# Kernel tuning notes

Measured on AMD Instinct MI355X. Metric: run time of the kernel, lower is better.

The kernel has to match this reference:

```python
import jax, jax.numpy as jnp
import numpy as np

B, N, C, H, D, K = 4, 8192, 384, 12, 2, 256
M = N // K          # 32 members per cluster
CH = C // H         # 32 head dim


def setup_inputs() -> dict:
    key = jax.random.key(0)
    ks = jax.random.split(key, 8)
    pos = jax.random.uniform(ks[0], (B, N, D), jnp.float32) * 100.0
    feat = jax.random.normal(ks[1], (B, N, C), jnp.float32)
    # each batch's points partitioned into K clusters of M members (a permutation)
    perms = jax.vmap(lambda kk: jax.random.permutation(kk, N))(jax.random.split(ks[2], B))
    member_idx = perms.reshape(B * K, M).astype(jnp.int32)               # z x m
    batch_idx = jnp.broadcast_to(
        jnp.repeat(jnp.arange(B, dtype=jnp.int32), K)[:, None], (B * K, M))
    w = 0.02
    qkv_w = jax.random.normal(ks[3], (3 * C, C), jnp.float32) * w
    qkv_b = jnp.zeros((3 * C,), jnp.float32)
    pos_w = jax.random.normal(ks[4], (H, D), jnp.float32) * w
    pos_b = jnp.zeros((H,), jnp.float32)
    proj_w = jax.random.normal(ks[5], (C, C), jnp.float32) * w
    proj_b = jnp.zeros((C,), jnp.float32)
    return dict(pos=pos, feat=feat, member_idx=member_idx, batch_idx=batch_idx,
                qkv_w=qkv_w, qkv_b=qkv_b, pos_w=pos_w, pos_b=pos_b,
                proj_w=proj_w, proj_b=proj_b, k=K)


def reference(pos, feat, member_idx, batch_idx, qkv_w, qkv_b, pos_w, pos_b,
              proj_w, proj_b, k):
    # attend_means=True, mask=None, cluster_score=None, q_subsample_idx=None path
    b, n, c = feat.shape
    d = pos.shape[2]
    h = pos_w.shape[0]
    ch = c // h
    z, m = member_idx.shape
    scale = ch ** -0.5

    qkv = feat @ qkv_w.T + qkv_b            # b,n,3c
    q = qkv[..., :c]                        # b,n,c
    kv = qkv[..., c:]                       # b,n,2c

    pos_orig = pos
    pos_n = pos / jnp.max(pos.reshape(-1, d), axis=0)   # per-coordinate max norm

    # irregular gather of kv / pos per cluster member
    kv_g = kv[batch_idx, member_idx]        # z,m,2c
    pos_g = pos_n[batch_idx, member_idx]    # z,m,d

    # cluster_score=None, mask=None -> uniform weights 1/m (mean over members)
    kv_mean = jnp.mean(kv_g, axis=1).reshape(b, k, 2, h, ch)
    pos_mean = jnp.mean(pos_g, axis=1).reshape(b, k, d)

    key_ = kv_mean[:, :, 0].transpose(0, 2, 1, 3)   # b,h,k,ch
    v = kv_mean[:, :, 1].transpose(0, 2, 1, 3)      # b,h,k,ch
    qh = q.reshape(b, n, h, ch).transpose(0, 2, 1, 3) * scale  # b,h,n,ch

    attn = jnp.einsum('bhnc,bhkc->bhnk', qh, key_)  # b,h,n,k
    rel_pos = pos_mean[:, None, :, :] - pos_orig[:, :, None, :]  # b,n,k,d
    pos_bias = jnp.einsum('bnkd,hd->bhnk', rel_pos, pos_w) + pos_b[None, :, None, None]
    attn = jax.nn.softmax(attn + pos_bias, axis=-1)

    out = jnp.einsum('bhnk,bhkc->bnhc', attn, v).reshape(b, n, c)
    return out @ proj_w.T + proj_b
```

## Files before the change

### kernel.cpp

```cpp
#include <hip/hip_runtime.h>

typedef __attribute__((ext_vector_type(8))) short bf16x8;
typedef __attribute__((ext_vector_type(4))) float f32x4;

#define MFMA16(a,b,c) __builtin_amdgcn_mfma_f32_16x16x32_bf16((a),(b),(c),0,0,0)

__device__ __forceinline__ float b2f(unsigned short u){
  union { unsigned u; float f; } x; x.u = ((unsigned)u) << 16; return x.f;
}
__device__ __forceinline__ unsigned short f2b(float f){
  union { float f; unsigned u; } x; x.f = f;
  unsigned r = x.u + 0x7FFFu + ((x.u >> 16) & 1u);
  return (unsigned short)(r >> 16);
}
__device__ __forceinline__ unsigned pk_rne(float a, float b){
  unsigned ua = __float_as_uint(a), ub = __float_as_uint(b);
  ua += 0x7FFFu + ((ua >> 16) & 1u);
  ub += 0x7FFFu + ((ub >> 16) & 1u);
  return __builtin_amdgcn_perm(ub, ua, 0x07060302u);
}
__device__ __forceinline__ unsigned pk_trunc(float a, float b){
  return __builtin_amdgcn_perm(__float_as_uint(b), __float_as_uint(a), 0x07060302u);
}
__device__ __forceinline__ bf16x8 mk8(unsigned a, unsigned b, unsigned c, unsigned d){
  union { uint4 u; bf16x8 h; } x; x.u = make_uint4(a,b,c,d); return x.h;
}
__device__ __forceinline__ int permp(int cl){
  return (cl & 0xE0) | (((cl >> 2) & 3) << 3) | (((cl >> 4) & 1) << 2) | (cl & 3);
}

typedef __attribute__((address_space(3))) unsigned int lds_u32;
typedef const __attribute__((address_space(1))) unsigned int glb_u32;
__device__ __forceinline__ void gl_lds16(const void* g, void* l){
  __builtin_amdgcn_global_load_lds((glb_u32*)g, (lds_u32*)l, 16, 0, 0);
}

__global__ __launch_bounds__(256) void cvt_kernel(const float* __restrict__ in,
                                                  unsigned short* __restrict__ o, long n8){
  long i = (long)blockIdx.x*256 + threadIdx.x;
  if (i >= n8) return;
  const float4* p = (const float4*)(in + i*8);
  float4 a = p[0], b = p[1];
  *(uint4*)(o + i*8) = make_uint4(pk_rne(a.x,a.y), pk_rne(a.z,a.w),
                                  pk_rne(b.x,b.y), pk_rne(b.z,b.w));
}

__global__ __launch_bounds__(256) void posmax_kernel(const float* __restrict__ pos,
                                                     unsigned* __restrict__ pmax){
  int i = blockIdx.x*256 + threadIdx.x;
  float4 v = ((const float4*)pos)[i];
  float m0 = fmaxf(v.x, v.z), m1 = fmaxf(v.y, v.w);
  #pragma unroll
  for (int off = 32; off >= 1; off >>= 1){
    m0 = fmaxf(m0, __shfl_xor(m0, off, 64));
    m1 = fmaxf(m1, __shfl_xor(m1, off, 64));
  }
  if ((threadIdx.x & 63) == 0){
    atomicMax(&pmax[0], __float_as_uint(m0));
    atomicMax(&pmax[1], __float_as_uint(m1));
  }
}

__global__ __launch_bounds__(192) void cluster_means_kernel(
    const float* __restrict__ feat, const float* __restrict__ pos,
    const int* __restrict__ member_idx, const int* __restrict__ batch_idx,
    unsigned short* __restrict__ fm, float* __restrict__ pm)
{
  int z = blockIdx.x, t = threadIdx.x;
  __shared__ int bases[32];
  if (t < 32) bases[t] = batch_idx[z*32 + t]*8192 + member_idx[z*32 + t];
  __syncthreads();
  float a0 = 0.f, a1 = 0.f, p = 0.f;
  for (int m = 0; m < 32; m++){
    const float* row = feat + (long)bases[m]*384;
    a0 += row[t];
    a1 += row[t+192];
    if (t < 2) p += pos[(long)bases[m]*2 + t];
  }
  fm[(long)z*384 + t]       = f2b(a0 * (1.f/32.f));
  fm[(long)z*384 + t + 192] = f2b(a1 * (1.f/32.f));
  if (t < 2) pm[z*2 + t] = p * (1.f/32.f);
}

__global__ __launch_bounds__(256) void bias_kernel(
    const float* __restrict__ pm, const float* __restrict__ pmaxf,
    const float* __restrict__ pos_w, const float* __restrict__ pos_b,
    unsigned short* __restrict__ wt)
{
  int idx = blockIdx.x*256 + threadIdx.x;
  int kc = idx & 255;
  int bh = idx >> 8;
  int h = bh % 12;
  float p0 = pm[((bh/12)*256 + kc)*2]   / pmaxf[0];
  float p1 = pm[((bh/12)*256 + kc)*2+1] / pmaxf[1];
  float bias = p0*pos_w[h*2] + p1*pos_w[h*2+1] + pos_b[h];
  wt[(bh << 8) + permp(kc)] = f2b(exp2f(bias * 1.44269504088896340f));
}

__global__ __launch_bounds__(256) void gemm_kv_kernel(
    const unsigned short* __restrict__ A, const unsigned short* __restrict__ W,
    const float* __restrict__ bias, unsigned short* __restrict__ kh,
    unsigned short* __restrict__ vt, const unsigned short* __restrict__ wt)
{
  __shared__ unsigned short As[64*64];
  __shared__ unsigned short Ws[128*64];
  const int N = 768, K = 384;
  int mt = blockIdx.x / 6, nt = blockIdx.x - mt*6;
  int m0 = mt << 6, n0 = nt << 7;
  int tid = threadIdx.x;
  int lane = tid & 63, wave = tid >> 6;
  int wr = (wave >> 1) << 5, wc = (wave & 1) << 6;
  int l15 = lane & 15, quad = lane >> 4;
  int sw = l15 & 7;
  int srow = tid >> 3, sc8 = tid & 7;

  f32x4 acc[2][4];
  #pragma unroll
  for (int i = 0; i < 2; i++)
    #pragma unroll
    for (int j = 0; j < 4; j++) acc[i][j] = (f32x4){0.f,0.f,0.f,0.f};

  for (int k0 = 0; k0 < K; k0 += 64){
    __syncthreads();
    #pragma unroll
    for (int it = 0; it < 2; it++){
      int r = srow + it*32;
      int gc8 = sc8 ^ (r & 7);
      gl_lds16(A + (long)(m0+r)*K + k0 + gc8*8, As + it*2048 + wave*512);
    }
    #pragma unroll
    for (int it = 0; it < 4; it++){
      int r = srow + it*32;
      int gc8 = sc8 ^ (r & 7);
      gl_lds16(W + (long)(n0+r)*K + k0 + gc8*8, Ws + it*2048 + wave*512);
    }
    __syncthreads();
    #pragma unroll
    for (int kk = 0; kk < 2; kk++){
      bf16x8 af[2], bfr[4];
      #pragma unroll
      for (int i = 0; i < 2; i++)
        af[i] = *(const bf16x8*)(As + (wr + i*16 + l15)*64 + (((kk<<2)+quad) ^ sw)*8);
      #pragma unroll
      for (int j = 0; j < 4; j++)
        bfr[j] = *(const bf16x8*)(Ws + (wc + j*16 + l15)*64 + (((kk<<2)+quad) ^ sw)*8);
      #pragma unroll
      for (int i = 0; i < 2; i++)
        #pragma unroll
        for (int j = 0; j < 4; j++)
          acc[i][j] = MFMA16(af[i], bfr[j], acc[i][j]);
    }
  }

  #pragma unroll
  for (int j = 0; j < 4; j++){
    int col = n0 + wc + j*16 + l15;
    float bv = bias[col];
    #pragma unroll
    for (int i = 0; i < 2; i++){
      int row0 = m0 + wr + i*16 + quad*4;
      #pragma unroll
      for (int r = 0; r < 4; r++){
        float v = acc[i][j][r] + bv;
        int row = row0 + r;
        int b = row >> 8, cl = row & 255;
        if (col < 384){
          int h = col >> 5, ch = col & 31;
          kh[((((long)b*12 + h)*256 + cl)*32) + ch] = f2b(v);
        } else {
          int cn = col - 384;
          int h = cn >> 5, ch = cn & 31;
          int pp = permp(cl);
          int c8 = (pp >> 3) ^ (ch & 7);
          float w = b2f(wt[(((long)b*12 + h) << 8) + pp]);
          vt[(((long)b*12 + h)*32 + ch)*256 + c8*8 + (pp & 7)] = f2b(v * w);
        }
      }
    }
  }
}

template<int OUT_F32, int AF32>
__global__ __launch_bounds__(256) void gemm_fn_kernel(
    const void* __restrict__ Av, const unsigned short* __restrict__ W,
    const float* __restrict__ bias, void* __restrict__ Cv, float out_scale)
{
  __shared__ unsigned short As[64*72];
  __shared__ unsigned short Ws[384*64];
  const int K = 384, N = 384;
  int m0 = blockIdx.x << 6;
  int tid = threadIdx.x;
  int lane = tid & 63, wave = tid >> 6;
  int l15 = lane & 15, quad = lane >> 4;
  int sw = l15 & 7;
  int srow = tid >> 3, sc8 = tid & 7;

  f32x4 acc[4][6];
  #pragma unroll
  for (int i = 0; i < 4; i++)
    #pragma unroll
    for (int j = 0; j < 6; j++) acc[i][j] = (f32x4){0.f,0.f,0.f,0.f};

  for (int k0 = 0; k0 < K; k0 += 64){
    __syncthreads();
    if (AF32){
      const float* Af = (const float*)Av;
      #pragma unroll
      for (int it = 0; it < 4; it++){
        int r = (tid >> 4) + it*16;
        int c4 = tid & 15;
        float4 v = *(const float4*)(Af + (long)(m0+r)*K + k0 + c4*4);
        *(uint2*)(As + r*72 + c4*4) = make_uint2(pk_rne(v.x,v.y), pk_rne(v.z,v.w));
      }
    } else {
      const unsigned short* A = (const unsigned short*)Av;
      #pragma unroll
      for (int it = 0; it < 2; it++){
        int r = srow + it*32;
        int gc8 = sc8 ^ (r & 7);
        gl_lds16(A + (long)(m0+r)*K + k0 + gc8*8, As + it*2048 + wave*512);
      }
    }
    #pragma unroll
    for (int it = 0; it < 12; it++){
      int r = srow + it*32;
      int gc8 = sc8 ^ (r & 7);
      gl_lds16(W + (long)r*K + k0 + gc8*8, Ws + it*2048 + wave*512);
    }
    __syncthreads();
    #pragma unroll
    for (int kk = 0; kk < 2; kk++){
      bf16x8 af[4];
      #pragma unroll
      for (int i = 0; i < 4; i++){
        int r = i*16 + l15;
        if (AF32) af[i] = *(const bf16x8*)(As + r*72 + ((kk<<2)+quad)*8);
        else      af[i] = *(const bf16x8*)(As + r*64 + (((kk<<2)+quad) ^ sw)*8);
      }
      #pragma unroll
      for (int j = 0; j < 6; j++){
        bf16x8 bfr = *(const bf16x8*)(Ws + (wave*96 + j*16 + l15)*64 + (((kk<<2)+quad) ^ sw)*8);
        #pragma unroll
        for (int i = 0; i < 4; i++)
          acc[i][j] = MFMA16(af[i], bfr, acc[i][j]);
      }
    }
  }

  #pragma unroll
  for (int j = 0; j < 6; j++){
    int col = wave*96 + j*16 + l15;
    float bv = bias[col];
    #pragma unroll
    for (int i = 0; i < 4; i++){
      int row0 = m0 + i*16 + quad*4;
      #pragma unroll
      for (int r = 0; r < 4; r++){
        float v = (acc[i][j][r] + bv) * out_scale;
        if (OUT_F32) ((float*)Cv)[(long)(row0+r)*N + col] = v;
        else ((unsigned short*)Cv)[(long)(row0+r)*N + col] = f2b(v);
      }
    }
  }
}

__global__ __launch_bounds__(256) void attn_kernel(
    const unsigned short* __restrict__ qs,
    const unsigned short* __restrict__ kh,
    const unsigned short* __restrict__ vt,
    const unsigned short* __restrict__ wt,
    unsigned short* __restrict__ ao)
{
  __shared__ unsigned short keyS[256*32];
  __shared__ unsigned short vTS[32*256];
  __shared__ unsigned short wS[256];

  int bid = blockIdx.x;
  int chunk = bid & 127;
  int h = (bid >> 7) % 12;
  int b = bid / (128*12);
  int bh = b*12 + h;
  int n0 = chunk << 6;
  int tid = threadIdx.x, lane = tid & 63, wave = tid >> 6;
  int l15 = lane & 15, quad = lane >> 4;
  int sw = l15 & 7;

  const unsigned short* khb = kh + (long)bh*8192;
  const unsigned short* vtb = vt + (long)bh*8192;
  #pragma unroll
  for (int it = 0; it < 4; it++){
    gl_lds16(khb + it*2048 + tid*8, keyS + it*2048 + wave*512);
    gl_lds16(vtb + it*2048 + tid*8, vTS  + it*2048 + wave*512);
  }
  if (tid < 32) *(uint4*)(wS + tid*8) = *(const uint4*)(wt + ((long)bh << 8) + tid*8);
  __syncthreads();

  int tok0 = n0 + wave*16;
  bf16x8 aq = *(const bf16x8*)(qs + ((long)b*8192 + tok0 + l15)*384 + h*32 + quad*8);

  f32x4 S[16];
  #pragma unroll
  for (int kb = 0; kb < 16; kb++){
    bf16x8 bk = *(const bf16x8*)(keyS + (kb*16 + l15)*32 + quad*8);
    f32x4 z = {0.f,0.f,0.f,0.f};
    S[kb] = MFMA16(bk, aq, z);
  }

  #pragma unroll
  for (int kb = 0; kb < 16; kb++)
    #pragma unroll
    for (int c = 0; c < 4; c++) S[kb][c] = exp2f(S[kb][c]);

  f32x4 o0 = {0.f,0.f,0.f,0.f}, o1 = {0.f,0.f,0.f,0.f}, os = {0.f,0.f,0.f,0.f};
  #pragma unroll
  for (int ks = 0; ks < 8; ks++){
    bf16x8 pf = mk8(pk_trunc(S[2*ks][0],   S[2*ks][1]),
                    pk_trunc(S[2*ks][2],   S[2*ks][3]),
                    pk_trunc(S[2*ks+1][0], S[2*ks+1][1]),
                    pk_trunc(S[2*ks+1][2], S[2*ks+1][3]));
    int c8 = (4*ks + quad) ^ sw;
    bf16x8 a0 = *(const bf16x8*)(vTS + l15*256      + c8*8);
    bf16x8 a1 = *(const bf16x8*)(vTS + (16+l15)*256 + c8*8);
    bf16x8 wf = *(const bf16x8*)(wS + ks*32 + quad*8);
    o0 = MFMA16(a0, pf, o0);
    o1 = MFMA16(a1, pf, o1);
    os = MFMA16(wf, pf, os);
  }
  float inv = 1.f / os[0];
  long obase = ((long)b*8192 + tok0 + l15)*384 + h*32 + quad*4;
  unsigned q0 = pk_rne(o0[0]*inv, o0[1]*inv), q1 = pk_rne(o0[2]*inv, o0[3]*inv);
  unsigned q2 = pk_rne(o1[0]*inv, o1[1]*inv), q3 = pk_rne(o1[2]*inv, o1[3]*inv);
  *(uint2*)(ao + obase)      = make_uint2(q0, q1);
  *(uint2*)(ao + obase + 16) = make_uint2(q2, q3);
}

extern "C" void kernel_launch(void* const* d_in, const int* in_sizes, int n_in,
                              void* d_out, int out_size, void* d_ws, size_t ws_size,
                              hipStream_t stream)
{
  const float* pos      = (const float*)d_in[0];
  const float* feat     = (const float*)d_in[1];
  const int* member_idx = (const int*)d_in[2];
  const int* batch_idx  = (const int*)d_in[3];
  const float* qkv_w    = (const float*)d_in[4];
  const float* qkv_b    = (const float*)d_in[5];
  const float* pos_w    = (const float*)d_in[6];
  const float* pos_b    = (const float*)d_in[7];
  const float* proj_w   = (const float*)d_in[8];
  const float* proj_b   = (const float*)d_in[9];
  float* out = (float*)d_out;

  char* ws = (char*)d_ws;
  float* pmax           = (float*)ws;
  float* pm             = (float*)(ws + 256);
  unsigned short* fm    = (unsigned short*)(ws + 8704);
  unsigned short* kh    = (unsigned short*)(ws + 795136);
  unsigned short* vt    = (unsigned short*)(ws + 1581568);
  unsigned short* wt    = (unsigned short*)(ws + 2368000);
  unsigned short* q_s   = (unsigned short*)(ws + 2417152);
  unsigned short* ao    = (unsigned short*)(ws + 27582976);
  unsigned short* qkvwb = (unsigned short*)(ws + 52748800);
  unsigned short* projwb= (unsigned short*)(ws + 53633536);

  hipMemsetAsync(pmax, 0, 8, stream);
  posmax_kernel<<<64, 256, 0, stream>>>(pos, (unsigned*)pmax);
  cvt_kernel<<<216, 256, 0, stream>>>(qkv_w, qkvwb, 55296);
  cvt_kernel<<<72, 256, 0, stream>>>(proj_w, projwb, 18432);
  cluster_means_kernel<<<1024, 192, 0, stream>>>(feat, pos, member_idx, batch_idx, fm, pm);
  bias_kernel<<<48, 256, 0, stream>>>(pm, pmax, pos_w, pos_b, wt);
  gemm_kv_kernel<<<96, 256, 0, stream>>>(fm, qkvwb + 384*384, qkv_b + 384, kh, vt, wt);
  gemm_fn_kernel<0,1><<<512, 256, 0, stream>>>(feat, qkvwb, qkv_b, q_s,
                                               0.17677669529663687f * 1.44269504088896340f);
  attn_kernel<<<6144, 256, 0, stream>>>(q_s, kh, vt, wt, ao);
  gemm_fn_kernel<1,0><<<512, 256, 0, stream>>>(ao, projwb, proj_b, out, 1.0f);
}
```

Baseline: 226.1 us.

## Persistent attention blocks, smaller GEMM k-tile, vectorized cluster-mean gather

The attention kernel now launches one block per (batch, head, 512-token slice) and loops over 8 token chunks. This amortizes the shared-memory load of the key/value tiles, and the next chunk's q fragment is prefetched during the current one. The GEMM k-tile shrinks from 64 to 32 with a 4-way swizzle, cutting LDS footprint to raise occupancy at the cost of twice as many barriers. Cluster means now process two clusters per block using float4 loads and packed bf16 stores.

```diff
diff --git a/kernel.cpp b/kernel.cpp
--- a/kernel.cpp
+++ b/kernel.cpp
@@ -66,20 +66,26 @@
     const int* __restrict__ member_idx, const int* __restrict__ batch_idx,
     unsigned short* __restrict__ fm, float* __restrict__ pm)
 {
-  int z = blockIdx.x, t = threadIdx.x;
-  __shared__ int bases[32];
-  if (t < 32) bases[t] = batch_idx[z*32 + t]*8192 + member_idx[z*32 + t];
+  int t = threadIdx.x;
+  int g = t / 96, tl = t - g*96;
+  int z = blockIdx.x*2 + g;
+  __shared__ int bases[2][32];
+  if (tl < 32) bases[g][tl] = batch_idx[z*32 + tl]*8192 + member_idx[z*32 + tl];
   __syncthreads();
-  float a0 = 0.f, a1 = 0.f, p = 0.f;
+  float4 a = {0.f,0.f,0.f,0.f};
+  float p = 0.f;
+  const float4* f4 = (const float4*)feat;
+  #pragma unroll 4
   for (int m = 0; m < 32; m++){
-    const float* row = feat + (long)bases[m]*384;
-    a0 += row[t];
-    a1 += row[t+192];
-    if (t < 2) p += pos[(long)bases[m]*2 + t];
-  }
-  fm[(long)z*384 + t]       = f2b(a0 * (1.f/32.f));
-  fm[(long)z*384 + t + 192] = f2b(a1 * (1.f/32.f));
-  if (t < 2) pm[z*2 + t] = p * (1.f/32.f);
+    int row = bases[g][m];
+    float4 v = f4[(long)row*96 + tl];
+    a.x += v.x; a.y += v.y; a.z += v.z; a.w += v.w;
+    if (tl < 2) p += pos[(long)row*2 + tl];
+  }
+  unsigned d0 = pk_rne(a.x*(1.f/32.f), a.y*(1.f/32.f));
+  unsigned d1 = pk_rne(a.z*(1.f/32.f), a.w*(1.f/32.f));
+  *(uint2*)(fm + (long)z*384 + tl*4) = make_uint2(d0, d1);
+  if (tl < 2) pm[z*2 + tl] = p * (1.f/32.f);
 }
 
 __global__ __launch_bounds__(256) void bias_kernel(
@@ -185,15 +191,15 @@
     const void* __restrict__ Av, const unsigned short* __restrict__ W,
     const float* __restrict__ bias, void* __restrict__ Cv, float out_scale)
 {
-  __shared__ unsigned short As[64*72];
-  __shared__ unsigned short Ws[384*64];
+  __shared__ unsigned short As[64*32];
+  __shared__ unsigned short Ws[384*32];
   const int K = 384, N = 384;
   int m0 = blockIdx.x << 6;
   int tid = threadIdx.x;
   int lane = tid & 63, wave = tid >> 6;
   int l15 = lane & 15, quad = lane >> 4;
-  int sw = l15 & 7;
-  int srow = tid >> 3, sc8 = tid & 7;
+  int sw3 = l15 & 3;
+  int sr = tid >> 2, sc = tid & 3;
 
   f32x4 acc[4][6];
   #pragma unroll
@@ -201,49 +207,37 @@
     #pragma unroll
     for (int j = 0; j < 6; j++) acc[i][j] = (f32x4){0.f,0.f,0.f,0.f};
 
-  for (int k0 = 0; k0 < K; k0 += 64){
+  for (int k0 = 0; k0 < K; k0 += 32){
     __syncthreads();
     if (AF32){
       const float* Af = (const float*)Av;
-      #pragma unroll
-      for (int it = 0; it < 4; it++){
-        int r = (tid >> 4) + it*16;
-        int c4 = tid & 15;
-        float4 v = *(const float4*)(Af + (long)(m0+r)*K + k0 + c4*4);
-        *(uint2*)(As + r*72 + c4*4) = make_uint2(pk_rne(v.x,v.y), pk_rne(v.z,v.w));
-      }
+      int gc = sc ^ (sr & 3);
+      const float4* src = (const float4*)(Af + (long)(m0+sr)*K + k0 + gc*8);
+      float4 v0 = src[0], v1 = src[1];
+      *(uint4*)(As + sr*32 + sc*8) = make_uint4(pk_rne(v0.x,v0.y), pk_rne(v0.z,v0.w),
+                                                pk_rne(v1.x,v1.y), pk_rne(v1.z,v1.w));
     } else {
       const unsigned short* A = (const unsigned short*)Av;
-      #pragma unroll
-      for (int it = 0; it < 2; it++){
-        int r = srow + it*32;
-        int gc8 = sc8 ^ (r & 7);
-        gl_lds16(A + (long)(m0+r)*K + k0 + gc8*8, As + it*2048 + wave*512);
-      }
-    }
-    #pragma unroll
-    for (int it = 0; it < 12; it++){
-      int r = srow + it*32;
-      int gc8 = sc8 ^ (r & 7);
-      gl_lds16(W + (long)r*K + k0 + gc8*8, Ws + it*2048 + wave*512);
+      int gc = sc ^ (sr & 3);
+      gl_lds16(A + (long)(m0+sr)*K + k0 + gc*8, As + wave*512);
+    }
+    #pragma unroll
+    for (int it = 0; it < 6; it++){
+      int r = it*64 + sr;
+      int gc = sc ^ (r & 3);
+      gl_lds16(W + (long)r*K + k0 + gc*8, Ws + it*2048 + wave*512);
     }
     __syncthreads();
-    #pragma unroll
-    for (int kk = 0; kk < 2; kk++){
-      bf16x8 af[4];
-      #pragma unroll
-      for (int i = 0; i < 4; i++){
-        int r = i*16 + l15;
-        if (AF32) af[i] = *(const bf16x8*)(As + r*72 + ((kk<<2)+quad)*8);
-        else      af[i] = *(const bf16x8*)(As + r*64 + (((kk<<2)+quad) ^ sw)*8);
-      }
-      #pragma unroll
-      for (int j = 0; j < 6; j++){
-        bf16x8 bfr = *(const bf16x8*)(Ws + (wave*96 + j*16 + l15)*64 + (((kk<<2)+quad) ^ sw)*8);
-        #pragma unroll
-        for (int i = 0; i < 4; i++)
-          acc[i][j] = MFMA16(af[i], bfr, acc[i][j]);
-      }
+    bf16x8 af[4];
+    #pragma unroll
+    for (int i = 0; i < 4; i++)
+      af[i] = *(const bf16x8*)(As + (i*16 + l15)*32 + (quad ^ sw3)*8);
+    #pragma unroll
+    for (int j = 0; j < 6; j++){
+      bf16x8 bfr = *(const bf16x8*)(Ws + (wave*96 + j*16 + l15)*32 + (quad ^ sw3)*8);
+      #pragma unroll
+      for (int i = 0; i < 4; i++)
+        acc[i][j] = MFMA16(af[i], bfr, acc[i][j]);
     }
   }
 
@@ -276,11 +270,10 @@
   __shared__ unsigned short wS[256];
 
   int bid = blockIdx.x;
-  int chunk = bid & 127;
-  int h = (bid >> 7) % 12;
-  int b = bid / (128*12);
-  int bh = b*12 + h;
-  int n0 = chunk << 6;
+  int part = bid & 15;
+  int bh = bid >> 4;
+  int h = bh % 12;
+  int b = bh / 12;
   int tid = threadIdx.x, lane = tid & 63, wave = tid >> 6;
   int l15 = lane & 15, quad = lane >> 4;
   int sw = l15 & 7;
@@ -293,45 +286,52 @@
     gl_lds16(vtb + it*2048 + tid*8, vTS  + it*2048 + wave*512);
   }
   if (tid < 32) *(uint4*)(wS + tid*8) = *(const uint4*)(wt + ((long)bh << 8) + tid*8);
+
+  const unsigned short* qrow = qs + ((long)b*8192 + part*512 + wave*16 + l15)*384 + h*32 + quad*8;
+  unsigned short* aorow = ao + ((long)b*8192 + part*512 + wave*16 + l15)*384 + h*32 + quad*4;
+
+  bf16x8 aq = *(const bf16x8*)qrow;
   __syncthreads();
 
-  int tok0 = n0 + wave*16;
-  bf16x8 aq = *(const bf16x8*)(qs + ((long)b*8192 + tok0 + l15)*384 + h*32 + quad*8);
-
-  f32x4 S[16];
-  #pragma unroll
-  for (int kb = 0; kb < 16; kb++){
-    bf16x8 bk = *(const bf16x8*)(keyS + (kb*16 + l15)*32 + quad*8);
-    f32x4 z = {0.f,0.f,0.f,0.f};
-    S[kb] = MFMA16(bk, aq, z);
-  }
-
-  #pragma unroll
-  for (int kb = 0; kb < 16; kb++)
-    #pragma unroll
-    for (int c = 0; c < 4; c++) S[kb][c] = exp2f(S[kb][c]);
-
-  f32x4 o0 = {0.f,0.f,0.f,0.f}, o1 = {0.f,0.f,0.f,0.f}, os = {0.f,0.f,0.f,0.f};
-  #pragma unroll
-  for (int ks = 0; ks < 8; ks++){
-    bf16x8 pf = mk8(pk_trunc(S[2*ks][0],   S[2*ks][1]),
-                    pk_trunc(S[2*ks][2],   S[2*ks][3]),
-                    pk_trunc(S[2*ks+1][0], S[2*ks+1][1]),
-                    pk_trunc(S[2*ks+1][2], S[2*ks+1][3]));
-    int c8 = (4*ks + quad) ^ sw;
-    bf16x8 a0 = *(const bf16x8*)(vTS + l15*256      + c8*8);
-    bf16x8 a1 = *(const bf16x8*)(vTS + (16+l15)*256 + c8*8);
-    bf16x8 wf = *(const bf16x8*)(wS + ks*32 + quad*8);
-    o0 = MFMA16(a0, pf, o0);
-    o1 = MFMA16(a1, pf, o1);
-    os = MFMA16(wf, pf, os);
-  }
-  float inv = 1.f / os[0];
-  long obase = ((long)b*8192 + tok0 + l15)*384 + h*32 + quad*4;
-  unsigned q0 = pk_rne(o0[0]*inv, o0[1]*inv), q1 = pk_rne(o0[2]*inv, o0[3]*inv);
-  unsigned q2 = pk_rne(o1[0]*inv, o1[1]*inv), q3 = pk_rne(o1[2]*inv, o1[3]*inv);
-  *(uint2*)(ao + obase)      = make_uint2(q0, q1);
-  *(uint2*)(ao + obase + 16) = make_uint2(q2, q3);
+  for (int j = 0; j < 8; j++){
+    int jn = (j < 7) ? j + 1 : j;
+    bf16x8 aqn = *(const bf16x8*)(qrow + (long)jn*64*384);
+
+    f32x4 S[16];
+    #pragma unroll
+    for (int kb = 0; kb < 16; kb++){
+      bf16x8 bk = *(const bf16x8*)(keyS + (kb*16 + l15)*32 + quad*8);
+      f32x4 z = {0.f,0.f,0.f,0.f};
+      S[kb] = MFMA16(bk, aq, z);
+    }
+    #pragma unroll
+    for (int kb = 0; kb < 16; kb++)
+      #pragma unroll
+      for (int c = 0; c < 4; c++) S[kb][c] = exp2f(S[kb][c]);
+
+    f32x4 o0 = {0.f,0.f,0.f,0.f}, o1 = {0.f,0.f,0.f,0.f}, os = {0.f,0.f,0.f,0.f};
+    #pragma unroll
+    for (int ks = 0; ks < 8; ks++){
+      bf16x8 pf = mk8(pk_trunc(S[2*ks][0],   S[2*ks][1]),
+                      pk_trunc(S[2*ks][2],   S[2*ks][3]),
+                      pk_trunc(S[2*ks+1][0], S[2*ks+1][1]),
+                      pk_trunc(S[2*ks+1][2], S[2*ks+1][3]));
+      int c8 = (4*ks + quad) ^ sw;
+      bf16x8 a0 = *(const bf16x8*)(vTS + l15*256      + c8*8);
+      bf16x8 a1 = *(const bf16x8*)(vTS + (16+l15)*256 + c8*8);
+      bf16x8 wf = *(const bf16x8*)(wS + ks*32 + quad*8);
+      o0 = MFMA16(a0, pf, o0);
+      o1 = MFMA16(a1, pf, o1);
+      os = MFMA16(wf, pf, os);
+    }
+    float inv = 1.f / os[0];
+    unsigned short* aop = aorow + (long)j*64*384;
+    unsigned q0 = pk_rne(o0[0]*inv, o0[1]*inv), q1 = pk_rne(o0[2]*inv, o0[3]*inv);
+    unsigned q2 = pk_rne(o1[0]*inv, o1[1]*inv), q3 = pk_rne(o1[2]*inv, o1[3]*inv);
+    *(uint2*)(aop)      = make_uint2(q0, q1);
+    *(uint2*)(aop + 16) = make_uint2(q2, q3);
+    aq = aqn;
+  }
 }
 
 extern "C" void kernel_launch(void* const* d_in, const int* in_sizes, int n_in,
@@ -366,11 +366,11 @@
   posmax_kernel<<<64, 256, 0, stream>>>(pos, (unsigned*)pmax);
   cvt_kernel<<<216, 256, 0, stream>>>(qkv_w, qkvwb, 55296);
   cvt_kernel<<<72, 256, 0, stream>>>(proj_w, projwb, 18432);
-  cluster_means_kernel<<<1024, 192, 0, stream>>>(feat, pos, member_idx, batch_idx, fm, pm);
+  cluster_means_kernel<<<512, 192, 0, stream>>>(feat, pos, member_idx, batch_idx, fm, pm);
   bias_kernel<<<48, 256, 0, stream>>>(pm, pmax, pos_w, pos_b, wt);
   gemm_kv_kernel<<<96, 256, 0, stream>>>(fm, qkvwb + 384*384, qkv_b + 384, kh, vt, wt);
   gemm_fn_kernel<0,1><<<512, 256, 0, stream>>>(feat, qkvwb, qkv_b, q_s,
                                                0.17677669529663687f * 1.44269504088896340f);
-  attn_kernel<<<6144, 256, 0, stream>>>(q_s, kh, vt, wt, ao);
+  attn_kernel<<<768, 256, 0, stream>>>(q_s, kh, vt, wt, ao);
   gemm_fn_kernel<1,0><<<512, 256, 0, stream>>>(ao, projwb, proj_b, out, 1.0f);
 }
```

Result: slower. 244.4 us (+8.1%).
